# Kernel optimization log

Hardware: AMD Instinct MI355X
Metric: run time of the kernel (lower is better)

Reference implementation:

```python
import jax, jax.numpy as jnp
import numpy as np

B, S, D = 2, 2048, 512
WIN = 64  # local causal window (includes current token)
EPS = 1e-5


def setup_inputs() -> dict:
    key = jax.random.key(0)
    ks = jax.random.split(key, 8)
    sc = 0.02
    return {
        "x":  jax.random.normal(ks[0], (B, S, D), jnp.float32),
        "Wq": jax.random.normal(ks[1], (D, D), jnp.float32) * sc,
        "bq": jnp.zeros((D,), jnp.float32),
        "Wk": jax.random.normal(ks[2], (D, D), jnp.float32) * sc,
        "bk": jnp.zeros((D,), jnp.float32),
        "Wv": jax.random.normal(ks[3], (D, D), jnp.float32) * sc,
        "bv": jnp.zeros((D,), jnp.float32),
        "Wo": jax.random.normal(ks[4], (D, D), jnp.float32) * sc,
        "bo": jnp.zeros((D,), jnp.float32),
        "Wr": jax.random.normal(ks[5], (D, D), jnp.float32) * sc,
        "br": jnp.zeros((D,), jnp.float32),
        "gamma": jnp.ones((D,), jnp.float32),
        "beta":  jnp.zeros((D,), jnp.float32),
    }


def _layernorm(h, gamma, beta):
    mu = jnp.mean(h, axis=-1, keepdims=True)
    var = jnp.mean(jnp.square(h - mu), axis=-1, keepdims=True)
    return (h - mu) * jax.lax.rsqrt(var + EPS) * gamma + beta


def _local_attention(x, Wq, bq, Wk, bk, Wv, bv, Wo, bo):
    q = x @ Wq + bq
    k = x @ Wk + bk
    v = x @ Wv + bv
    kp = jnp.pad(k, ((0, 0), (WIN - 1, 0), (0, 0)))
    vp = jnp.pad(v, ((0, 0), (WIN - 1, 0), (0, 0)))
    idx = jnp.arange(S)[:, None] + jnp.arange(WIN)[None, :]
    kw = kp[:, idx, :]
    vw = vp[:, idx, :]
    scores = jnp.einsum('bsd,bswd->bsw', q, kw) / np.float32(np.sqrt(D))
    valid = (idx >= (WIN - 1 - jnp.zeros((), jnp.int32)))  # padded slots invalid
    valid = idx >= (WIN - 1) - jnp.arange(S)[:, None] * 0
    valid = (idx - (WIN - 1)) >= 0  # key position in original seq >= 0
    scores = jnp.where(valid[None, :, :], scores, jnp.float32(-1e9))
    attn = jax.nn.softmax(scores, axis=-1)
    out = jnp.einsum('bsw,bswd->bsd', attn, vw)
    return out @ Wo + bo


def reference(x, Wq, bq, Wk, bk, Wv, bv, Wo, bo, Wr, br, gamma, beta):
    read = _local_attention(x, Wq, bq, Wk, bk, Wv, bv, Wo, bo)
    sence = x @ Wr + br
    read = _layernorm(read, gamma, beta)
    sence = _layernorm(sence, gamma, beta)
    return jax.nn.gelu(read + sence, approximate=False)
```

## Files before the change

### kernel.cpp

```cpp
#include <hip/hip_runtime.h>
#include <hip/hip_bf16.h>
#include <math.h>

#define BB 2
#define SS 2048
#define DD 512
#define MTOT 4096

typedef __attribute__((ext_vector_type(8))) short sv8;
typedef __attribute__((ext_vector_type(4))) float f32x4;

static const size_t OFF_XB   = 0;
static const size_t OFF_WT   = 4194304;
static const size_t OFF_BIAS = 6815744;
static const size_t OFF_Y    = 6823936;
static const size_t OFF_VT   = 19406848;
static const size_t OFF_READ = 23601152;
static const size_t OFF_PP   = 27795456;
static const size_t OFF_ATT  = 0;

static __device__ __forceinline__ float bf2f(short s) {
    unsigned u = ((unsigned)(unsigned short)s) << 16;
    return __builtin_bit_cast(float, u);
}
static __device__ __forceinline__ short f2bf(float f) {
    unsigned u = __builtin_bit_cast(unsigned, f);
    unsigned r = 0x7fffu + ((u >> 16) & 1u);
    u += r;
    return (short)(u >> 16);
}

#define GLOAD_LDS16(gp, lp)                                                        \
    __builtin_amdgcn_global_load_lds(                                              \
        (const __attribute__((address_space(1))) unsigned*)(gp),                   \
        (__attribute__((address_space(3))) unsigned*)(lp), 16, 0, 0)

__global__ __launch_bounds__(256) void cast_x(const float* __restrict__ x,
                                              short* __restrict__ xb, int n4) {
    int i = blockIdx.x * 256 + threadIdx.x;
    if (i < n4) {
        float4 v = ((const float4*)x)[i];
        short4 o;
        o.x = f2bf(v.x); o.y = f2bf(v.y); o.z = f2bf(v.z); o.w = f2bf(v.w);
        ((short4*)xb)[i] = o;
    }
}

__global__ __launch_bounds__(256) void prep_all(const float* __restrict__ Wq,
                                                const float* __restrict__ Wk,
                                                const float* __restrict__ Wv,
                                                const float* __restrict__ Wr,
                                                const float* __restrict__ Wo,
                                                const float* __restrict__ bq,
                                                const float* __restrict__ bk,
                                                const float* __restrict__ bv,
                                                const float* __restrict__ br,
                                                short* __restrict__ wt,
                                                float* __restrict__ ball) {
    int z = blockIdx.z;
    if (z == 5) {
        if (blockIdx.y != 0 || blockIdx.x >= 8) return;
        int i = blockIdx.x * 256 + threadIdx.x;
        int sel = i >> 9;
        const float* src = (sel == 0) ? bq : (sel == 1) ? bk : (sel == 2) ? bv : br;
        ball[i] = src[i & 511];
        return;
    }
    __shared__ float tile[32][33];
    const float* W = (z == 0) ? Wq : (z == 1) ? Wk : (z == 2) ? Wv : (z == 3) ? Wr : Wo;
    int k0 = blockIdx.y * 32, n0 = blockIdx.x * 32;
    int tx = threadIdx.x & 31, ty = threadIdx.x >> 5;
    for (int r = ty; r < 32; r += 8)
        tile[r][tx] = W[(size_t)(k0 + r) * 512 + n0 + tx];
    __syncthreads();
    short* o = wt + (size_t)z * 512 * 512;
    for (int r = ty; r < 32; r += 8)
        o[(size_t)(n0 + r) * 512 + k0 + tx] = f2bf(tile[tx][r]);
}

template <int GEMM1>
__global__ __launch_bounds__(256) void gemm_bt(const short* __restrict__ A,
                                               const short* __restrict__ Bt,
                                               const float* __restrict__ bias,
                                               short* __restrict__ Cout, int ldc,
                                               short* __restrict__ vt) {
    __shared__ __align__(16) short lA[128 * 64];
    __shared__ __align__(16) short lB[128 * 64];
    int tid = threadIdx.x;
    int mbase = blockIdx.y * 128;
    int nbase = blockIdx.x * 128;
    int lane = tid & 63, wave = tid >> 6;
    int wm = wave >> 1, wn = wave & 1;
    bool vswap = GEMM1 && (nbase >= 1024) && (nbase < 1536);

    f32x4 acc[4][4] = {};

    int srow = (lane >> 3);
    int scol = (lane & 7) * 8;

    for (int k0 = 0; k0 < 512; k0 += 64) {
#pragma unroll
        for (int c = 0; c < 4; ++c) {
            int ch = wave * 4 + c;
            int row = ch * 8 + srow;
            GLOAD_LDS16(A + (size_t)(mbase + row) * 512 + k0 + scol, &lA[ch * 512]);
            GLOAD_LDS16(Bt + (size_t)(nbase + row) * 512 + k0 + scol, &lB[ch * 512]);
        }
        __syncthreads();
#pragma unroll
        for (int kk = 0; kk < 2; ++kk) {
            int koff = kk * 32 + (lane >> 4) * 8;
            sv8 af[4], bfr[4];
#pragma unroll
            for (int m = 0; m < 4; ++m)
                af[m] = *(const sv8*)&lA[(wm * 64 + m * 16 + (lane & 15)) * 64 + koff];
#pragma unroll
            for (int n = 0; n < 4; ++n)
                bfr[n] = *(const sv8*)&lB[(wn * 64 + n * 16 + (lane & 15)) * 64 + koff];
            if (!vswap) {
#pragma unroll
                for (int m = 0; m < 4; ++m)
#pragma unroll
                    for (int n = 0; n < 4; ++n)
                        acc[m][n] = __builtin_amdgcn_mfma_f32_16x16x32_bf16(
                            af[m], bfr[n], acc[m][n], 0, 0, 0);
            } else {
#pragma unroll
                for (int m = 0; m < 4; ++m)
#pragma unroll
                    for (int n = 0; n < 4; ++n)
                        acc[m][n] = __builtin_amdgcn_mfma_f32_16x16x32_bf16(
                            bfr[n], af[m], acc[m][n], 0, 0, 0);
            }
        }
        __syncthreads();
    }

    int r0 = (lane >> 4) * 4, c0 = lane & 15;
    if (!vswap) {
#pragma unroll
        for (int m = 0; m < 4; ++m)
#pragma unroll
            for (int n = 0; n < 4; ++n) {
                int col = nbase + wn * 64 + n * 16 + c0;
                float bv = bias[col];
                int ycol = (GEMM1 && col >= 1536) ? col - 512 : col;
#pragma unroll
                for (int j = 0; j < 4; ++j) {
                    int row = mbase + wm * 64 + m * 16 + r0 + j;
                    Cout[(size_t)row * ldc + ycol] = f2bf(acc[m][n][j] + bv);
                }
            }
    } else {
        int bb = mbase >> 11, tb = mbase & 2047;
#pragma unroll
        for (int m = 0; m < 4; ++m)
#pragma unroll
            for (int n = 0; n < 4; ++n) {
                int dglob = nbase + wn * 64 + n * 16 + r0;
                int d = dglob - 1024;
                int tl = tb + wm * 64 + m * 16 + c0;
#pragma unroll
                for (int j = 0; j < 4; ++j) {
                    float v = acc[m][n][j] + bias[dglob + j];
                    vt[((size_t)bb * 512 + d + j) * 2048 + tl] = f2bf(v);
                }
            }
    }
}

__global__ __launch_bounds__(256) void attn_scores(const short* __restrict__ Y,
                                                   short* __restrict__ Pp) {
    __shared__ float sS[64][132];
    int tile = blockIdx.x;
    int b = tile >> 5;
    int t0 = (tile & 31) * 64;
    int s0 = tile * 64;
    int tid = threadIdx.x, lane = tid & 63, wave = tid >> 6;
    int wm = wave >> 1, wn = wave & 1;

    f32x4 acc[2][4] = {};
    const short* Q = Y;
    const short* Kb = Y + 512;

    int arow[2], brow[4];
#pragma unroll
    for (int m = 0; m < 2; ++m) arow[m] = s0 + wm * 32 + m * 16 + (lane & 15);
#pragma unroll
    for (int n = 0; n < 4; ++n) {
        int kr = t0 - 64 + wn * 64 + n * 16 + (lane & 15);
        if (kr < 0) kr = 0;
        brow[n] = (b << 11) + kr;
    }
#pragma unroll
    for (int step = 0; step < 16; ++step) {
        int koff = step * 32 + (lane >> 4) * 8;
        sv8 af[2], bfr[4];
#pragma unroll
        for (int m = 0; m < 2; ++m)
            af[m] = *(const sv8*)(Q + (size_t)arow[m] * 1536 + koff);
#pragma unroll
        for (int n = 0; n < 4; ++n)
            bfr[n] = *(const sv8*)(Kb + (size_t)brow[n] * 1536 + koff);
#pragma unroll
        for (int m = 0; m < 2; ++m)
#pragma unroll
            for (int n = 0; n < 4; ++n)
                acc[m][n] = __builtin_amdgcn_mfma_f32_16x16x32_bf16(
                    af[m], bfr[n], acc[m][n], 0, 0, 0);
    }
    int r0 = (lane >> 4) * 4, c0 = lane & 15;
#pragma unroll
    for (int m = 0; m < 2; ++m)
#pragma unroll
        for (int n = 0; n < 4; ++n) {
            int jc = wn * 64 + n * 16 + c0;
#pragma unroll
            for (int j = 0; j < 4; ++j)
                sS[wm * 32 + m * 16 + r0 + j][jc] =
                    acc[m][n][j] * 0.04419417382415922f;
        }
    __syncthreads();

    int q = tid >> 2, j0 = (tid & 3) * 32;
    float v[32];
    float mx = -1e30f;
    int jlo = q + 1;
    int jmin0 = 64 - t0;
    if (jmin0 > jlo) jlo = jmin0;
    int jhi = q + 64;
#pragma unroll
    for (int jj = 0; jj < 32; ++jj) {
        int j = j0 + jj;
        bool ok = (j >= jlo) && (j <= jhi);
        float s = ok ? sS[q][j] : -1e30f;
        v[jj] = s;
        mx = fmaxf(mx, s);
    }
    mx = fmaxf(mx, __shfl_xor(mx, 1));
    mx = fmaxf(mx, __shfl_xor(mx, 2));
    float sum = 0.f;
#pragma unroll
    for (int jj = 0; jj < 32; ++jj) {
        float e = (v[jj] > -1e29f) ? __expf(v[jj] - mx) : 0.f;
        v[jj] = e;
        sum += e;
    }
    sum += __shfl_xor(sum, 1);
    sum += __shfl_xor(sum, 2);
    float inv = 1.f / sum;
    short* dst = Pp + (size_t)tile * 8192 + q * 128 + j0;
#pragma unroll
    for (int k = 0; k < 4; ++k) {
        sv8 o;
#pragma unroll
        for (int e = 0; e < 8; ++e) o[e] = f2bf(v[k * 8 + e] * inv);
        *(sv8*)(dst + k * 8) = o;
    }
}

__global__ __launch_bounds__(256) void attn_pv(const short* __restrict__ Pp,
                                               const short* __restrict__ Vt,
                                               short* __restrict__ att) {
    int tile = blockIdx.y, dchunk = blockIdx.x;
    int b = tile >> 5;
    int t0 = (tile & 31) * 64;
    int s0 = tile * 64;
    int tid = threadIdx.x, lane = tid & 63, wave = tid >> 6;
    int wm = wave >> 1, wn = wave & 1;

    f32x4 acc[2][4] = {};
    const short* Pbase = Pp + (size_t)tile * 8192;
#pragma unroll
    for (int ks = 0; ks < 4; ++ks) {
        int koff = ks * 32 + (lane >> 4) * 8;
        sv8 af[2], bfr[4];
#pragma unroll
        for (int m = 0; m < 2; ++m)
            af[m] = *(const sv8*)(Pbase + (wm * 32 + m * 16 + (lane & 15)) * 128 + koff);
#pragma unroll
        for (int n = 0; n < 4; ++n) {
            int d = dchunk * 128 + wn * 64 + n * 16 + (lane & 15);
            long off = (long)(b * 512 + d) * 2048 + (t0 - 64 + koff);
            bfr[n] = *(const sv8*)(Vt + off);
        }
#pragma unroll
        for (int m = 0; m < 2; ++m)
#pragma unroll
            for (int n = 0; n < 4; ++n)
                acc[m][n] = __builtin_amdgcn_mfma_f32_16x16x32_bf16(
                    af[m], bfr[n], acc[m][n], 0, 0, 0);
    }
    int r0 = (lane >> 4) * 4, c0 = lane & 15;
#pragma unroll
    for (int m = 0; m < 2; ++m)
#pragma unroll
        for (int n = 0; n < 4; ++n) {
            int col = dchunk * 128 + wn * 64 + n * 16 + c0;
#pragma unroll
            for (int j = 0; j < 4; ++j) {
                int row = s0 + wm * 32 + m * 16 + r0 + j;
                att[(size_t)row * 512 + col] = f2bf(acc[m][n][j]);
            }
        }
}

__global__ __launch_bounds__(256) void ln_gelu(const short* __restrict__ readb,
                                               const short* __restrict__ Y,
                                               const float* __restrict__ gamma,
                                               const float* __restrict__ beta,
                                               float* __restrict__ out) {
    int s = blockIdx.x;
    int tid = threadIdx.x;
    const short* r = readb + (size_t)s * 512;
    const short* sn = Y + (size_t)s * 1536 + 1024;
    float r0 = bf2f(r[tid]), r1 = bf2f(r[tid + 256]);
    float s0 = bf2f(sn[tid]), s1 = bf2f(sn[tid + 256]);

    float v0 = r0 + r1, v1 = r0 * r0 + r1 * r1;
    float v2 = s0 + s1, v3 = s0 * s0 + s1 * s1;
#pragma unroll
    for (int off = 32; off; off >>= 1) {
        v0 += __shfl_xor(v0, off);
        v1 += __shfl_xor(v1, off);
        v2 += __shfl_xor(v2, off);
        v3 += __shfl_xor(v3, off);
    }
    __shared__ float red[4][4];
    int wave = tid >> 6, lane = tid & 63;
    if (lane == 0) {
        red[wave][0] = v0; red[wave][1] = v1; red[wave][2] = v2; red[wave][3] = v3;
    }
    __syncthreads();
    float t0 = red[0][0] + red[1][0] + red[2][0] + red[3][0];
    float t1 = red[0][1] + red[1][1] + red[2][1] + red[3][1];
    float t2 = red[0][2] + red[1][2] + red[2][2] + red[3][2];
    float t3 = red[0][3] + red[1][3] + red[2][3] + red[3][3];

    float mu_r = t0 * (1.f / 512.f);
    float var_r = t1 * (1.f / 512.f) - mu_r * mu_r;
    float is_r = rsqrtf(var_r + 1e-5f);
    float mu_s = t2 * (1.f / 512.f);
    float var_s = t3 * (1.f / 512.f) - mu_s * mu_s;
    float is_s = rsqrtf(var_s + 1e-5f);

    float g0 = gamma[tid], be0 = beta[tid];
    float g1 = gamma[tid + 256], be1 = beta[tid + 256];
    float x0 = (r0 - mu_r) * is_r * g0 + be0 + (s0 - mu_s) * is_s * g0 + be0;
    float x1 = (r1 - mu_r) * is_r * g1 + be1 + (s1 - mu_s) * is_s * g1 + be1;
    float y0 = 0.5f * x0 * (1.f + erff(x0 * 0.70710678118654752f));
    float y1 = 0.5f * x1 * (1.f + erff(x1 * 0.70710678118654752f));
    out[(size_t)s * 512 + tid] = y0;
    out[(size_t)s * 512 + tid + 256] = y1;
}

extern "C" void kernel_launch(void* const* d_in, const int* in_sizes, int n_in,
                              void* d_out, int out_size, void* d_ws, size_t ws_size,
                              hipStream_t stream) {
    const float* x  = (const float*)d_in[0];
    const float* Wq = (const float*)d_in[1];
    const float* bq = (const float*)d_in[2];
    const float* Wk = (const float*)d_in[3];
    const float* bk = (const float*)d_in[4];
    const float* Wv = (const float*)d_in[5];
    const float* bv = (const float*)d_in[6];
    const float* Wo = (const float*)d_in[7];
    const float* bo = (const float*)d_in[8];
    const float* Wr = (const float*)d_in[9];
    const float* br = (const float*)d_in[10];
    const float* gamma = (const float*)d_in[11];
    const float* beta  = (const float*)d_in[12];

    char* ws = (char*)d_ws;
    short* xb    = (short*)(ws + OFF_XB);
    short* wt    = (short*)(ws + OFF_WT);
    float* ball  = (float*)(ws + OFF_BIAS);
    short* Y     = (short*)(ws + OFF_Y);
    short* vtb   = (short*)(ws + OFF_VT);
    short* readb = (short*)(ws + OFF_READ);
    short* Pp    = (short*)(ws + OFF_PP);
    short* att   = (short*)(ws + OFF_ATT);

    cast_x<<<2048, 256, 0, stream>>>(x, xb, MTOT * DD / 4);
    prep_all<<<dim3(16, 16, 6), 256, 0, stream>>>(Wq, Wk, Wv, Wr, Wo, bq, bk, bv, br,
                                                  wt, ball);

    gemm_bt<1><<<dim3(16, 32), 256, 0, stream>>>(xb, wt, ball, Y, 1536, vtb);

    attn_scores<<<64, 256, 0, stream>>>(Y, Pp);
    attn_pv<<<dim3(4, 64), 256, 0, stream>>>(Pp, vtb, att);

    gemm_bt<0><<<dim3(4, 32), 256, 0, stream>>>(att, wt + (size_t)4 * 512 * 512, bo,
                                                readb, 512, nullptr);

    ln_gelu<<<4096, 256, 0, stream>>>(readb, Y, gamma, beta, (float*)d_out);
}
```

Measured before the change: 157.2 us.

## Fuse x cast into prep, stage GEMM epilogue via LDS, wave-per-row LayerNorm

Folds the fp32-to-bf16 cast of x into the weight-prep kernel, which removes one launch. The GEMM epilogue now writes tiles to LDS and then stores them to global memory as 16-byte vectors, replacing scattered 2-byte stores. The LN+GELU kernel assigns one wave per row with vector loads and a shuffle-only reduction, dropping the shared-memory reduction and the block barrier. The cast now runs on only 256 blocks, and the epilogue adds an extra barrier and an LDS round trip.

```diff
diff --git a/kernel.cpp b/kernel.cpp
--- a/kernel.cpp
+++ b/kernel.cpp
@@ -35,18 +35,8 @@
         (const __attribute__((address_space(1))) unsigned*)(gp),                   \
         (__attribute__((address_space(3))) unsigned*)(lp), 16, 0, 0)
 
-__global__ __launch_bounds__(256) void cast_x(const float* __restrict__ x,
-                                              short* __restrict__ xb, int n4) {
-    int i = blockIdx.x * 256 + threadIdx.x;
-    if (i < n4) {
-        float4 v = ((const float4*)x)[i];
-        short4 o;
-        o.x = f2bf(v.x); o.y = f2bf(v.y); o.z = f2bf(v.z); o.w = f2bf(v.w);
-        ((short4*)xb)[i] = o;
-    }
-}
-
-__global__ __launch_bounds__(256) void prep_all(const float* __restrict__ Wq,
+__global__ __launch_bounds__(256) void prep_all(const float* __restrict__ x,
+                                                const float* __restrict__ Wq,
                                                 const float* __restrict__ Wk,
                                                 const float* __restrict__ Wv,
                                                 const float* __restrict__ Wr,
@@ -55,21 +45,34 @@
                                                 const float* __restrict__ bk,
                                                 const float* __restrict__ bv,
                                                 const float* __restrict__ br,
+                                                short* __restrict__ xb,
                                                 short* __restrict__ wt,
                                                 float* __restrict__ ball) {
     int z = blockIdx.z;
+    int tid = threadIdx.x;
     if (z == 5) {
-        if (blockIdx.y != 0 || blockIdx.x >= 8) return;
-        int i = blockIdx.x * 256 + threadIdx.x;
-        int sel = i >> 9;
-        const float* src = (sel == 0) ? bq : (sel == 1) ? bk : (sel == 2) ? bv : br;
-        ball[i] = src[i & 511];
+        int flat = blockIdx.y * 16 + blockIdx.x;
+        if (flat == 0) {
+#pragma unroll
+            for (int it = 0; it < 8; ++it) {
+                int i = it * 256 + tid;
+                int sel = i >> 9;
+                const float* src = (sel == 0) ? bq : (sel == 1) ? bk : (sel == 2) ? bv : br;
+                ball[i] = src[i & 511];
+            }
+        }
+        for (int i = flat * 256 + tid; i < MTOT * DD / 4; i += 256 * 256) {
+            float4 v = ((const float4*)x)[i];
+            short4 o;
+            o.x = f2bf(v.x); o.y = f2bf(v.y); o.z = f2bf(v.z); o.w = f2bf(v.w);
+            ((short4*)xb)[i] = o;
+        }
         return;
     }
     __shared__ float tile[32][33];
     const float* W = (z == 0) ? Wq : (z == 1) ? Wk : (z == 2) ? Wv : (z == 3) ? Wr : Wo;
     int k0 = blockIdx.y * 32, n0 = blockIdx.x * 32;
-    int tx = threadIdx.x & 31, ty = threadIdx.x >> 5;
+    int tx = tid & 31, ty = tid >> 5;
     for (int r = ty; r < 32; r += 8)
         tile[r][tx] = W[(size_t)(k0 + r) * 512 + n0 + tx];
     __syncthreads();
@@ -84,8 +87,9 @@
                                                const float* __restrict__ bias,
                                                short* __restrict__ Cout, int ldc,
                                                short* __restrict__ vt) {
-    __shared__ __align__(16) short lA[128 * 64];
-    __shared__ __align__(16) short lB[128 * 64];
+    __shared__ __align__(16) short lbuf[2 * 128 * 64];
+    short* lA = lbuf;
+    short* lB = lbuf + 128 * 64;
     int tid = threadIdx.x;
     int mbase = blockIdx.y * 128;
     int nbase = blockIdx.x * 128;
@@ -138,19 +142,28 @@
 
     int r0 = (lane >> 4) * 4, c0 = lane & 15;
     if (!vswap) {
+        short* sC = lbuf;
 #pragma unroll
         for (int m = 0; m < 4; ++m)
 #pragma unroll
             for (int n = 0; n < 4; ++n) {
-                int col = nbase + wn * 64 + n * 16 + c0;
-                float bv = bias[col];
-                int ycol = (GEMM1 && col >= 1536) ? col - 512 : col;
+                int cl = wn * 64 + n * 16 + c0;
+                float bv = bias[nbase + cl];
 #pragma unroll
                 for (int j = 0; j < 4; ++j) {
-                    int row = mbase + wm * 64 + m * 16 + r0 + j;
-                    Cout[(size_t)row * ldc + ycol] = f2bf(acc[m][n][j] + bv);
+                    int rl = wm * 64 + m * 16 + r0 + j;
+                    sC[rl * 128 + cl] = f2bf(acc[m][n][j] + bv);
                 }
             }
+        __syncthreads();
+        int nybase = (GEMM1 && nbase >= 1536) ? nbase - 512 : nbase;
+#pragma unroll
+        for (int it = 0; it < 8; ++it) {
+            int idx = it * 256 + tid;
+            int row = idx >> 4, slot = idx & 15;
+            sv8 v = *(const sv8*)&sC[row * 128 + slot * 8];
+            *(sv8*)&Cout[(size_t)(mbase + row) * ldc + nybase + slot * 8] = v;
+        }
     } else {
         int bb = mbase >> 11, tb = mbase & 2047;
 #pragma unroll
@@ -310,48 +323,47 @@
                                                const float* __restrict__ gamma,
                                                const float* __restrict__ beta,
                                                float* __restrict__ out) {
-    int s = blockIdx.x;
-    int tid = threadIdx.x;
-    const short* r = readb + (size_t)s * 512;
-    const short* sn = Y + (size_t)s * 1536 + 1024;
-    float r0 = bf2f(r[tid]), r1 = bf2f(r[tid + 256]);
-    float s0 = bf2f(sn[tid]), s1 = bf2f(sn[tid + 256]);
-
-    float v0 = r0 + r1, v1 = r0 * r0 + r1 * r1;
-    float v2 = s0 + s1, v3 = s0 * s0 + s1 * s1;
+    int row = blockIdx.x * 4 + (threadIdx.x >> 6);
+    int lane = threadIdx.x & 63;
+    sv8 rv = *(const sv8*)(readb + (size_t)row * 512 + lane * 8);
+    sv8 sv = *(const sv8*)(Y + (size_t)row * 1536 + 1024 + lane * 8);
+    float rf[8], sf[8];
+    float sr = 0.f, sr2 = 0.f, ss = 0.f, ss2 = 0.f;
+#pragma unroll
+    for (int e = 0; e < 8; ++e) {
+        rf[e] = bf2f(rv[e]); sf[e] = bf2f(sv[e]);
+        sr += rf[e]; sr2 += rf[e] * rf[e];
+        ss += sf[e]; ss2 += sf[e] * sf[e];
+    }
 #pragma unroll
     for (int off = 32; off; off >>= 1) {
-        v0 += __shfl_xor(v0, off);
-        v1 += __shfl_xor(v1, off);
-        v2 += __shfl_xor(v2, off);
-        v3 += __shfl_xor(v3, off);
-    }
-    __shared__ float red[4][4];
-    int wave = tid >> 6, lane = tid & 63;
-    if (lane == 0) {
-        red[wave][0] = v0; red[wave][1] = v1; red[wave][2] = v2; red[wave][3] = v3;
-    }
-    __syncthreads();
-    float t0 = red[0][0] + red[1][0] + red[2][0] + red[3][0];
-    float t1 = red[0][1] + red[1][1] + red[2][1] + red[3][1];
-    float t2 = red[0][2] + red[1][2] + red[2][2] + red[3][2];
-    float t3 = red[0][3] + red[1][3] + red[2][3] + red[3][3];
-
-    float mu_r = t0 * (1.f / 512.f);
-    float var_r = t1 * (1.f / 512.f) - mu_r * mu_r;
-    float is_r = rsqrtf(var_r + 1e-5f);
-    float mu_s = t2 * (1.f / 512.f);
-    float var_s = t3 * (1.f / 512.f) - mu_s * mu_s;
-    float is_s = rsqrtf(var_s + 1e-5f);
-
-    float g0 = gamma[tid], be0 = beta[tid];
-    float g1 = gamma[tid + 256], be1 = beta[tid + 256];
-    float x0 = (r0 - mu_r) * is_r * g0 + be0 + (s0 - mu_s) * is_s * g0 + be0;
-    float x1 = (r1 - mu_r) * is_r * g1 + be1 + (s1 - mu_s) * is_s * g1 + be1;
-    float y0 = 0.5f * x0 * (1.f + erff(x0 * 0.70710678118654752f));
-    float y1 = 0.5f * x1 * (1.f + erff(x1 * 0.70710678118654752f));
-    out[(size_t)s * 512 + tid] = y0;
-    out[(size_t)s * 512 + tid + 256] = y1;
+        sr += __shfl_xor(sr, off);
+        sr2 += __shfl_xor(sr2, off);
+        ss += __shfl_xor(ss, off);
+        ss2 += __shfl_xor(ss2, off);
+    }
+    float mu_r = sr * (1.f / 512.f);
+    float is_r = rsqrtf(sr2 * (1.f / 512.f) - mu_r * mu_r + 1e-5f);
+    float mu_s = ss * (1.f / 512.f);
+    float is_s = rsqrtf(ss2 * (1.f / 512.f) - mu_s * mu_s + 1e-5f);
+
+    float4 ga = ((const float4*)gamma)[lane * 2];
+    float4 gb = ((const float4*)gamma)[lane * 2 + 1];
+    float4 ba = ((const float4*)beta)[lane * 2];
+    float4 bb = ((const float4*)beta)[lane * 2 + 1];
+    float g[8] = {ga.x, ga.y, ga.z, ga.w, gb.x, gb.y, gb.z, gb.w};
+    float be[8] = {ba.x, ba.y, ba.z, ba.w, bb.x, bb.y, bb.z, bb.w};
+
+    float y[8];
+#pragma unroll
+    for (int e = 0; e < 8; ++e) {
+        float xv = (rf[e] - mu_r) * is_r * g[e] + be[e] +
+                   (sf[e] - mu_s) * is_s * g[e] + be[e];
+        y[e] = 0.5f * xv * (1.f + erff(xv * 0.70710678118654752f));
+    }
+    float* o = out + (size_t)row * 512 + lane * 8;
+    ((float4*)o)[0] = make_float4(y[0], y[1], y[2], y[3]);
+    ((float4*)o)[1] = make_float4(y[4], y[5], y[6], y[7]);
 }
 
 extern "C" void kernel_launch(void* const* d_in, const int* in_sizes, int n_in,
@@ -381,9 +393,8 @@
     short* Pp    = (short*)(ws + OFF_PP);
     short* att   = (short*)(ws + OFF_ATT);
 
-    cast_x<<<2048, 256, 0, stream>>>(x, xb, MTOT * DD / 4);
-    prep_all<<<dim3(16, 16, 6), 256, 0, stream>>>(Wq, Wk, Wv, Wr, Wo, bq, bk, bv, br,
-                                                  wt, ball);
+    prep_all<<<dim3(16, 16, 6), 256, 0, stream>>>(x, Wq, Wk, Wv, Wr, Wo,
+                                                  bq, bk, bv, br, xb, wt, ball);
 
     gemm_bt<1><<<dim3(16, 32), 256, 0, stream>>>(xb, wt, ball, Y, 1536, vtb);
 
@@ -393,5 +404,5 @@
     gemm_bt<0><<<dim3(4, 32), 256, 0, stream>>>(att, wt + (size_t)4 * 512 * 512, bo,
                                                 readb, 512, nullptr);
 
-    ln_gelu<<<4096, 256, 0, stream>>>(readb, Y, gamma, beta, (float*)d_out);
-}
+    ln_gelu<<<1024, 256, 0, stream>>>(readb, Y, gamma, beta, (float*)d_out);
+}
```

Result: no change. 154.3 us (-1.9%).
